# Optimization experiments

Measured on AMD Instinct MI355X. Metric: run time of the kernel, lower is better.

Reference implementation:

```python
import jax, jax.numpy as jnp
import numpy as np

ANG = 9        # angRes (forced by hardcoded center index 40 -> 81 views)
MINDISP = -4
MAXDISP = 4


def setup_inputs() -> dict:
    key = jax.random.key(0)
    k1, k2 = jax.random.split(key)
    x = jax.random.normal(k1, (2, 4, 81, 96, 96), dtype=jnp.float32)
    mask = jax.random.uniform(k2, (2, 81, 96, 96), dtype=jnp.float32)
    return {"x": x, "mask": mask}


def _build_cost(x, mask):
    # Faithful translation of BuildCost.forward.
    # The chain of (ZeroPad2d on each view) -> (macro-image rearrange) ->
    # (crop) -> (Unfold kernel=A, dilation=(h_pad-d, w_pad-d)) -> (mask
    # modulate) -> (Unfold2) is algebraically a per-view shifted gather:
    #   cost[b,d,p,q,ck,u,v] = x_padview[b,ck,u,v, p+off(d,u), q+off(d,v)]
    #                          * mask[b, u*A+v, p, q]
    # with off(d,t) = (A//2)*(d-mindisp) - t*d, on views zero-padded by
    # bdr = (A//2)*maxdisp. Unfold2 is a pure reshape of the modulated
    # unfold columns. All indices stay inside each padded view.
    A, mind, maxd = ANG, MINDISP, MAXDISP
    b, c, aa, h, w = x.shape
    ctr = x[:, :, 40:41, :, :]                       # [b, c, 1, h, w]
    c0 = A // 2
    bdr = c0 * maxd
    xv = x.reshape(b, c, A, A, h, w)
    xp = jnp.pad(xv, ((0, 0), (0, 0), (0, 0), (0, 0), (bdr, bdr), (bdr, bdr)))
    D = maxd - mind + 1
    d = jnp.arange(mind, maxd + 1)                   # [D]
    uv = jnp.arange(A)                               # [A]
    off = c0 * (d[:, None] - mind) - uv[None, :] * d[:, None]   # [D, A]
    ridx = off[:, :, None] + jnp.arange(h)[None, None, :]       # [D, A, h]
    cidx = off[:, :, None] + jnp.arange(w)[None, None, :]       # [D, A, w]
    ui = uv[None, :, None, None, None]               # broadcast to [D,A,A,h,w]
    vi = uv[None, None, :, None, None]
    ri = ridx[:, :, None, :, None]
    ci = cidx[:, None, :, None, :]
    # g[b, c, D, u, v, p, q]
    g = xp[:, :, ui, vi, ri, ci]
    m = mask.reshape(b, 1, 1, A, A, h, w)            # mask channel a = u*A+v
    cost = g * m
    # torch output layout: [b, D, (p*w+q)*c + ck, u*A+v]
    cost = cost.transpose(0, 2, 5, 6, 1, 3, 4).reshape(b, D, h * w * c, A * A)
    return cost, ctr


def reference(x, mask):
    return _build_cost(x, mask)
```

## Files before the change

### kernel.cpp

```cpp
#include <hip/hip_runtime.h>


#define NAA 81
#define H 96
#define W 96
#define NC 4
#define ND 9
#define PLANE 9216
#define CHUNK 108
#define LSTR 97
#define WITHIN 324
#define OUTROW 31104
#define CTR_OFF 53747712LL

__global__ __launch_bounds__(512)
void build_cost_kernel(const float* __restrict__ x, const float* __restrict__ mask,
                       float* __restrict__ out) {
    __shared__ float xs[CHUNK * LSTR];
    __shared__ int   xbT[CHUNK];
    __shared__ int   mbT[CHUNK];
    __shared__ int   shT[CHUNK];
    __shared__ unsigned sh4[27];

    const int ii  = blockIdx.x;
    const int dd  = blockIdx.y;
    const int zz  = blockIdx.z;
    const int b   = zz / 3;
    const int k   = zz - 3 * b;
    const int d   = dd - 4;
    const int tid = threadIdx.x;

    if (tid < CHUNK) {
        int row = CHUNK * k + tid;
        int c  = row / 81;
        int uv = row - 81 * c;
        int u  = uv / 9;
        int v  = uv - 9 * u;
        int ri = ii + d * (4 - u);
        int xb = ((b * NC + c) * NAA + uv) * PLANE + ri * W;
        xbT[tid] = ((unsigned)ri < (unsigned)H) ? xb : -1;
        mbT[tid] = ((b * NAA + uv) * H + ii) * W;
        shT[tid] = d * (4 - v);
    }
    if (tid < 27) {
        unsigned p = 0;
        #pragma unroll
        for (int w = 0; w < 4; ++w) {
            int within = CHUNK * k + 4 * tid + w;
            int uv = within % 81;
            int v  = uv % 9;
            p |= (unsigned)(d * (4 - v) + 16) << (8 * w);
        }
        sh4[tid] = p;
    }
    __syncthreads();

    for (int idx = tid; idx < CHUNK * 24; idx += 512) {
        int rl = idx / 24;
        int cq = idx - rl * 24;
        int xb = xbT[rl];
        int mb = mbT[rl];
        int sh = shT[rl];
        int xbc = max(xb, 0);
        float* lrow = xs + rl * LSTR;
        #pragma unroll
        for (int g = 0; g < 4; ++g) {
            int col = cq + 24 * g;
            float xv = x[xbc + col];
            int jm = col - sh;
            float mv = mask[mb + min(max(jm, 0), W - 1)];
            float val = ((unsigned)jm < (unsigned)W && xb >= 0) ? xv * mv : 0.0f;
            lrow[col] = val;
        }
    }
    __syncthreads();

    const size_t gbase = (size_t)((b * ND + dd) * H + ii) * OUTROW + CHUNK * k;
    for (int G = tid; G < 96 * 27; G += 512) {
        int j = G / 27;
        int g = G - 27 * j;
        unsigned wp = sh4[g];
        float4 o;
        #pragma unroll
        for (int i = 0; i < 4; ++i) {
            int s   = (int)((wp >> (8 * i)) & 255u) - 16;
            int col = j + s;
            float val = xs[(4 * g + i) * LSTR + min(max(col, 0), W - 1)];
            (&o.x)[i] = ((unsigned)col < (unsigned)W) ? val : 0.0f;
        }
        *(float4*)(out + gbase + (size_t)j * WITHIN + 4 * g) = o;
    }

    if (dd == 4 && k == 0 && tid < 96) {
        int c = tid / 24;
        int q = tid - 24 * c;
        size_t so  = (size_t)((b * NC + c) * NAA + 40) * PLANE + (size_t)ii * W + 4 * q;
        size_t dst = CTR_OFF + (size_t)((b * NC + c) * H + ii) * W + 4 * q;
        *(float4*)(out + dst) = *(const float4*)(x + so);
    }
}

extern "C" void kernel_launch(void* const* d_in, const int* in_sizes, int n_in,
                              void* d_out, int out_size, void* d_ws, size_t ws_size,
                              hipStream_t stream) {
    const float* x    = (const float*)d_in[0];
    const float* mask = (const float*)d_in[1];
    float* out = (float*)d_out;
    dim3 grid(96, ND, 6);
    build_cost_kernel<<<grid, 512, 0, stream>>>(x, mask, out);
}
```

Baseline: 272.3 us.

## Split blocks by output column chunk with transposed LDS staging and nontemporal stores

Each block now covers all 324 (channel, view) rows for a 32-column slice of the output row, where before it covered a third of the rows across all 96 columns. Gathered x*mask products are staged in LDS transposed as [j][row], so the store phase is a flat, contiguous float4 copy to global memory. Stores use nontemporal hints. Row metadata is packed into a single lookup table. The cost is scattered, uncoalesced x loads (column index depends on a per-row shift), plus the redundant mask and x reads this pattern brings.

```diff
diff --git a/kernel.cpp b/kernel.cpp
--- a/kernel.cpp
+++ b/kernel.cpp
@@ -7,96 +7,97 @@
 #define NC 4
 #define ND 9
 #define PLANE 9216
-#define CHUNK 108
-#define LSTR 97
-#define WITHIN 324
+#define NR 324
+#define RS 328
+#define JB 32
 #define OUTROW 31104
 #define CTR_OFF 53747712LL
+
+typedef float f32x4 __attribute__((ext_vector_type(4)));
 
 __global__ __launch_bounds__(512)
 void build_cost_kernel(const float* __restrict__ x, const float* __restrict__ mask,
                        float* __restrict__ out) {
-    __shared__ float xs[CHUNK * LSTR];
-    __shared__ int   xbT[CHUNK];
-    __shared__ int   mbT[CHUNK];
-    __shared__ int   shT[CHUNK];
-    __shared__ unsigned sh4[27];
+    __shared__ __align__(16) float xs[JB * RS];
+    __shared__ __align__(16) int   lut[2 * NR];
 
     const int ii  = blockIdx.x;
     const int dd  = blockIdx.y;
     const int zz  = blockIdx.z;
     const int b   = zz / 3;
-    const int k   = zz - 3 * b;
+    const int jc  = zz - 3 * b;
+    const int j0  = JB * jc;
     const int d   = dd - 4;
     const int tid = threadIdx.x;
 
-    if (tid < CHUNK) {
-        int row = CHUNK * k + tid;
+    if (tid < NR) {
+        int row = tid;
         int c  = row / 81;
         int uv = row - 81 * c;
         int u  = uv / 9;
         int v  = uv - 9 * u;
         int ri = ii + d * (4 - u);
         int xb = ((b * NC + c) * NAA + uv) * PLANE + ri * W;
-        xbT[tid] = ((unsigned)ri < (unsigned)H) ? xb : -1;
-        mbT[tid] = ((b * NAA + uv) * H + ii) * W;
-        shT[tid] = d * (4 - v);
-    }
-    if (tid < 27) {
-        unsigned p = 0;
-        #pragma unroll
-        for (int w = 0; w < 4; ++w) {
-            int within = CHUNK * k + 4 * tid + w;
-            int uv = within % 81;
-            int v  = uv % 9;
-            p |= (unsigned)(d * (4 - v) + 16) << (8 * w);
-        }
-        sh4[tid] = p;
+        int mb = ((b * NAA + uv) * H + ii) * W;
+        int s  = d * (4 - v);
+        lut[2 * tid]     = ((unsigned)ri < (unsigned)H) ? xb : -1;
+        lut[2 * tid + 1] = (mb << 6) | (s + 16);
     }
     __syncthreads();
 
-    for (int idx = tid; idx < CHUNK * 24; idx += 512) {
-        int rl = idx / 24;
-        int cq = idx - rl * 24;
-        int xb = xbT[rl];
-        int mb = mbT[rl];
-        int sh = shT[rl];
-        int xbc = max(xb, 0);
-        float* lrow = xs + rl * LSTR;
-        #pragma unroll
-        for (int g = 0; g < 4; ++g) {
-            int col = cq + 24 * g;
-            float xv = x[xbc + col];
-            int jm = col - sh;
-            float mv = mask[mb + min(max(jm, 0), W - 1)];
-            float val = ((unsigned)jm < (unsigned)W && xb >= 0) ? xv * mv : 0.0f;
-            lrow[col] = val;
+    for (int idx = tid; idx < 81 * JB; idx += 512) {
+        int rq = idx >> 5;
+        int jj = idx & 31;
+        int j  = j0 + jj;
+        int4 P0 = *(const int4*)&lut[8 * rq];
+        int4 P1 = *(const int4*)&lut[8 * rq + 4];
+        float4 v;
+        {
+            int xb = P0.x, B = P0.y;
+            int s = (B & 63) - 16, col = j + s;
+            float xv = x[max(xb, 0) + min(max(col, 0), W - 1)];
+            float mv = mask[(B >> 6) + j];
+            v.x = (xb >= 0 && (unsigned)col < (unsigned)W) ? xv * mv : 0.0f;
         }
+        {
+            int xb = P0.z, B = P0.w;
+            int s = (B & 63) - 16, col = j + s;
+            float xv = x[max(xb, 0) + min(max(col, 0), W - 1)];
+            float mv = mask[(B >> 6) + j];
+            v.y = (xb >= 0 && (unsigned)col < (unsigned)W) ? xv * mv : 0.0f;
+        }
+        {
+            int xb = P1.x, B = P1.y;
+            int s = (B & 63) - 16, col = j + s;
+            float xv = x[max(xb, 0) + min(max(col, 0), W - 1)];
+            float mv = mask[(B >> 6) + j];
+            v.z = (xb >= 0 && (unsigned)col < (unsigned)W) ? xv * mv : 0.0f;
+        }
+        {
+            int xb = P1.z, B = P1.w;
+            int s = (B & 63) - 16, col = j + s;
+            float xv = x[max(xb, 0) + min(max(col, 0), W - 1)];
+            float mv = mask[(B >> 6) + j];
+            v.w = (xb >= 0 && (unsigned)col < (unsigned)W) ? xv * mv : 0.0f;
+        }
+        *(float4*)&xs[jj * RS + 4 * rq] = v;
     }
     __syncthreads();
 
-    const size_t gbase = (size_t)((b * ND + dd) * H + ii) * OUTROW + CHUNK * k;
-    for (int G = tid; G < 96 * 27; G += 512) {
-        int j = G / 27;
-        int g = G - 27 * j;
-        unsigned wp = sh4[g];
-        float4 o;
-        #pragma unroll
-        for (int i = 0; i < 4; ++i) {
-            int s   = (int)((wp >> (8 * i)) & 255u) - 16;
-            int col = j + s;
-            float val = xs[(4 * g + i) * LSTR + min(max(col, 0), W - 1)];
-            (&o.x)[i] = ((unsigned)col < (unsigned)W) ? val : 0.0f;
-        }
-        *(float4*)(out + gbase + (size_t)j * WITHIN + 4 * g) = o;
+    const size_t obase = (size_t)((b * ND + dd) * H + ii) * OUTROW + (size_t)j0 * NR;
+    for (int idx = tid; idx < 81 * JB; idx += 512) {
+        int j = idx / 81;
+        f32x4 v = *(const f32x4*)&xs[4 * (idx + j)];
+        __builtin_nontemporal_store(v, (f32x4*)(out + obase + 4 * (size_t)idx));
     }
 
-    if (dd == 4 && k == 0 && tid < 96) {
+    if (dd == 4 && jc == 0 && tid < 96) {
         int c = tid / 24;
         int q = tid - 24 * c;
         size_t so  = (size_t)((b * NC + c) * NAA + 40) * PLANE + (size_t)ii * W + 4 * q;
         size_t dst = CTR_OFF + (size_t)((b * NC + c) * H + ii) * W + 4 * q;
-        *(float4*)(out + dst) = *(const float4*)(x + so);
+        f32x4 cv = *(const f32x4*)(x + so);
+        __builtin_nontemporal_store(cv, (f32x4*)(out + dst));
     }
 }
 
```

Result: faster. 261.2 us (-4.1%).
